# Optimization experiments

Hardware: AMD Instinct MI355X
Metric: run time of the kernel (lower is better)

## Reference

```python
import jax, jax.numpy as jnp
import numpy as np

B, R, L = 1, 128, 256
IN_DIM, DM, DIM = 128, 32, 128  # in_dim, dim_msa, dim


def setup_inputs() -> dict:
    key = jax.random.key(0)
    k = jax.random.split(key, 6)
    x = jax.random.normal(k[0], (B, L, L, DIM), dtype=jnp.float32)
    m = jax.random.normal(k[1], (B, R, L, IN_DIM), dtype=jnp.float32)
    # proj_down1: Linear(in_dim -> dim_msa)
    W1 = jax.random.normal(k[2], (DM, IN_DIM), dtype=jnp.float32) * (1.0 / np.sqrt(IN_DIM))
    b1 = jax.random.normal(k[3], (DM,), dtype=jnp.float32) * 0.02
    # proj_down2: Linear(dim_msa**2 -> dim)
    W2 = jax.random.normal(k[4], (DIM, DM * DM), dtype=jnp.float32) * (1.0 / DM)
    b2 = jax.random.normal(k[5], (DIM,), dtype=jnp.float32) * 0.02
    return {"x": x, "m": m, "W1": W1, "b1": b1, "W2": W2, "b2": b2}


def reference(x, m, W1, b1, W2, b2):
    # proj_down1: [b, r, i, in_dim] -> [b, r, i, dim_msa]
    mp = jnp.einsum('brie,de->brid', m, W1) + b1
    nrows = mp.shape[1]
    # Original math: outer = einsum('brid,brjc->bijcd', mp, mp)/nrows,
    # then rearrange 'b i j c d -> b i j (c d)' and Linear(dm^2 -> dim).
    # Flattened index (c d) => W2[k, c*DM + d]; fuse projection into the
    # contraction so the huge [b,i,j,c,d] tensor is never materialized.
    W2r = W2.reshape(DIM, DM, DM)  # (k, c, d)
    outer = jnp.einsum('brid,brjc,kcd->bijk', mp, mp, W2r) / nrows + b2
    return x + outer
```

## Files before the change

kernel.cpp:

```cpp
#include <hip/hip_runtime.h>
#include <stdint.h>


typedef __attribute__((ext_vector_type(8))) short bf16x8;
typedef __attribute__((ext_vector_type(4))) float f32x4;

#define MFMA16 __builtin_amdgcn_mfma_f32_16x16x32_bf16

__device__ __forceinline__ unsigned short f2bf(float f) {
    union { float f; unsigned int u; } x; x.f = f;
    unsigned int r = (x.u + 0x7fffu + ((x.u >> 16) & 1u)) >> 16;
    return (unsigned short)r;
}

__device__ __forceinline__ bf16x8 load8f_bf(const float* p) {
    float4 v0 = *(const float4*)p;
    float4 v1 = *(const float4*)(p + 4);
    union { bf16x8 v; unsigned short u[8]; } r;
    r.u[0] = f2bf(v0.x); r.u[1] = f2bf(v0.y); r.u[2] = f2bf(v0.z); r.u[3] = f2bf(v0.w);
    r.u[4] = f2bf(v1.x); r.u[5] = f2bf(v1.y); r.u[6] = f2bf(v1.z); r.u[7] = f2bf(v1.w);
    return r.v;
}

__global__ __launch_bounds__(256) void prep_kernel(
    const float* __restrict__ m, const float* __restrict__ W1,
    const float* __restrict__ pb1, const float* __restrict__ W2,
    unsigned short* __restrict__ mpF, unsigned short* __restrict__ W2f)
{
    const int bx = blockIdx.x;
    if (bx >= 512) {
        const int t    = (bx - 512) * 256 + threadIdx.x;
        const int nt   = t >> 11;
        const int kc   = (t >> 6) & 31;
        const int lane = t & 63;
        const int ln   = lane & 15, q = lane >> 4;
        const float* src = W2 + (size_t)(nt * 16 + ln) * 1024 + kc;
        union { bf16x8 v; unsigned short u[8]; } r;
        #pragma unroll
        for (int j = 0; j < 8; ++j)
            r.u[j] = f2bf(src[(q * 8 + j) * 32]);
        *(bf16x8*)(W2f + (size_t)t * 8) = r.v;
        return;
    }
    const int lane = threadIdx.x & 63;
    const int w    = threadIdx.x >> 6;
    const int ln   = lane & 15, q = lane >> 4;
    const int tile = bx * 4 + w;
    const int i    = tile >> 3;
    const int r0   = (tile & 7) * 16;

    const float* Ap  = m  + ((size_t)(r0 + ln) * 256 + i) * 128 + q * 8;
    const float* Bp0 = W1 + (size_t)ln * 128 + q * 8;
    const float* Bp1 = W1 + (size_t)(16 + ln) * 128 + q * 8;

    f32x4 acc0 = {0.f, 0.f, 0.f, 0.f};
    f32x4 acc1 = {0.f, 0.f, 0.f, 0.f};
    #pragma unroll
    for (int ke = 0; ke < 4; ++ke) {
        bf16x8 a  = load8f_bf(Ap  + ke * 32);
        bf16x8 b0 = load8f_bf(Bp0 + ke * 32);
        bf16x8 b1 = load8f_bf(Bp1 + ke * 32);
        acc0 = MFMA16(a, b0, acc0, 0, 0, 0);
        acc1 = MFMA16(a, b1, acc1, 0, 0, 0);
    }
    const float bb0 = pb1[ln];
    const float bb1 = pb1[16 + ln];
    const int kr = r0 >> 5;
    const int qr = ((r0 >> 4) & 1) * 2 + (q >> 1);
    const int j0 = (q & 1) * 4;
    const size_t off0 = (size_t)(i * 2 + 0) * 2048 + kr * 512 + (qr * 16 + ln) * 8 + j0;
    const size_t off1 = (size_t)(i * 2 + 1) * 2048 + kr * 512 + (qr * 16 + ln) * 8 + j0;
    ushort4 o0, o1;
    o0.x = f2bf(acc0[0] + bb0); o0.y = f2bf(acc0[1] + bb0);
    o0.z = f2bf(acc0[2] + bb0); o0.w = f2bf(acc0[3] + bb0);
    o1.x = f2bf(acc1[0] + bb1); o1.y = f2bf(acc1[1] + bb1);
    o1.z = f2bf(acc1[2] + bb1); o1.w = f2bf(acc1[3] + bb1);
    *(ushort4*)(mpF + off0) = o0;
    *(ushort4*)(mpF + off1) = o1;
}

__device__ __forceinline__ void stepB(const unsigned short* __restrict__ Ab,
                                      const unsigned short* __restrict__ Bb,
                                      f32x4 (&acc)[2][4])
{
    #pragma unroll
    for (int a = 0; a < 2; ++a)
        #pragma unroll
        for (int b = 0; b < 4; ++b)
            acc[a][b] = (f32x4){0.f, 0.f, 0.f, 0.f};
    #pragma unroll
    for (int ks = 0; ks < 4; ++ks) {
        bf16x8 av[2], bv[4];
        av[0] = *(const bf16x8*)(Ab + ks * 512);
        av[1] = *(const bf16x8*)(Ab + 2048 + ks * 512);
        #pragma unroll
        for (int bn = 0; bn < 4; ++bn)
            bv[bn] = *(const bf16x8*)(Bb + bn * 4096 + ks * 512);
        #pragma unroll
        for (int am = 0; am < 2; ++am)
            #pragma unroll
            for (int bn = 0; bn < 4; ++bn)
                acc[am][bn] = MFMA16(av[am], bv[bn], acc[am][bn], 0, 0, 0);
    }
}

__device__ __forceinline__ void gwriteC(unsigned short* __restrict__ Gl,
                                        const f32x4 (&acc)[2][4],
                                        int ln, int q, int wm, int wn, int cbase)
{
    #pragma unroll
    for (int am = 0; am < 2; ++am) {
        const int chunk = cbase + ln * 4 + am * 2 + (q >> 1);
        const int sig   = chunk >> 3;
        const int hbase = chunk * 256 + (q & 1) * 4;
        #pragma unroll
        for (int bn = 0; bn < 4; ++bn) {
            const int p  = (wn * 4 + bn) * 4 + wm;
            const int pp = p ^ sig;
            ushort4 g;
            g.x = f2bf(acc[am][bn][0]); g.y = f2bf(acc[am][bn][1]);
            g.z = f2bf(acc[am][bn][2]); g.w = f2bf(acc[am][bn][3]);
            *(ushort4*)(Gl + hbase + pp * 8) = g;
        }
    }
}

__device__ __forceinline__ void wpre(const unsigned short* __restrict__ wp, bf16x8 (&wv)[8])
{
    #pragma unroll
    for (int k8 = 0; k8 < 8; ++k8)
        wv[k8] = *(const bf16x8*)(wp + k8 * 512);
}

__device__ __forceinline__ void stepC32(const unsigned short* __restrict__ Gl,
                                        const unsigned short* __restrict__ wp,
                                        bf16x8 (&wv)[8], int ln, int q,
                                        f32x4& c0, f32x4& c1)
{
    #pragma unroll
    for (int ks = 0; ks < 32; ++ks) {
        bf16x8 cur = wv[ks & 7];
        if (ks < 24) wv[ks & 7] = *(const bf16x8*)(wp + (ks + 8) * 512);
        const int chunk = ks * 4 + q;
        const int sig   = chunk >> 3;
        const unsigned short* gp = Gl + chunk * 256 + ((ln ^ sig) << 3);
        bf16x8 ag0 = *(const bf16x8*)gp;
        bf16x8 ag1 = *(const bf16x8*)(gp + 128);
        c0 = MFMA16(ag0, cur, c0, 0, 0, 0);
        c1 = MFMA16(ag1, cur, c1, 0, 0, 0);
    }
}

__global__ __launch_bounds__(512, 4) void fused_kernel(
    const float* __restrict__ x, const float* __restrict__ b2,
    const unsigned short* __restrict__ mpF, const unsigned short* __restrict__ W2f,
    float* __restrict__ out)
{
    __shared__ __align__(16) unsigned char smem[65536];
    unsigned short* Gl = (unsigned short*)smem;

    const int tid  = threadIdx.x;
    const int lane = tid & 63, w = tid >> 6;
    const int ln   = lane & 15, q = lane >> 4;
    const int wm   = w & 3, wn = w >> 2;

    const int i0 = blockIdx.x * 8;
    const int j0 = blockIdx.y * 8;

    const unsigned short* Ab0 = mpF + (size_t)((j0 + wm) * 2) * 2048 + lane * 8;
    const unsigned short* Ab1 = Ab0 + 16384;
    const unsigned short* Bb  = mpF + (size_t)((i0 + wn * 4) * 2) * 2048 + lane * 8;
    const unsigned short* wp0 = W2f + (size_t)(w * 32) * 512 + lane * 8;

    f32x4 cacc[4];
    #pragma unroll
    for (int t = 0; t < 4; ++t) cacc[t] = (f32x4){0.f, 0.f, 0.f, 0.f};
    f32x4 acc[2][4];
    bf16x8 wv[8];

    stepB(Ab0, Bb, acc);
    gwriteC(Gl, acc, ln, q, wm, wn, 0);
    stepB(Ab0, Bb + 2048, acc);
    gwriteC(Gl, acc, ln, q, wm, wn, 64);
    wpre(wp0, wv);
    __syncthreads();
    stepC32(Gl, wp0, wv, ln, q, cacc[0], cacc[1]);
    __syncthreads();

    stepB(Ab1, Bb, acc);
    gwriteC(Gl, acc, ln, q, wm, wn, 0);
    stepB(Ab1, Bb + 2048, acc);
    gwriteC(Gl, acc, ln, q, wm, wn, 64);
    wpre(wp0, wv);
    __syncthreads();

    float4 xv[4];
    size_t gb[4];
    #pragma unroll
    for (int e = 0; e < 4; ++e) {
        const int fid = e * 512 + tid;
        const int po  = fid >> 5, kq = fid & 31;
        gb[e] = ((size_t)(i0 + (po >> 3)) * 256 + (j0 + (po & 7))) * 128 + kq * 4;
        xv[e] = *(const float4*)(x + gb[e]);
    }

    stepC32(Gl, wp0, wv, ln, q, cacc[2], cacc[3]);
    __syncthreads();

    float* Ep = (float*)smem;
    const float invR = 1.0f / 128.0f;
    const int kk = w * 16 + ln;
    const int u  = kk >> 2, kl = kk & 3;
    #pragma unroll
    for (int jh = 0; jh < 2; ++jh)
        #pragma unroll
        for (int pt = 0; pt < 2; ++pt)
            #pragma unroll
            for (int rg = 0; rg < 4; ++rg) {
                const int po = (pt * 4 + q) * 8 + jh * 4 + rg;
                Ep[po * 128 + ((u ^ (po & 7)) << 2) + kl] = cacc[jh * 2 + pt][rg] * invR;
            }
    __syncthreads();

    #pragma unroll
    for (int e = 0; e < 4; ++e) {
        const int fid = e * 512 + tid;
        const int po  = fid >> 5, kq = fid & 31;
        const float4 v  = *(const float4*)(Ep + po * 128 + ((kq ^ (po & 7)) << 2));
        const float4 bv = *(const float4*)(b2 + kq * 4);
        float4 o;
        o.x = xv[e].x + v.x + bv.x; o.y = xv[e].y + v.y + bv.y;
        o.z = xv[e].z + v.z + bv.z; o.w = xv[e].w + v.w + bv.w;
        *(float4*)(out + gb[e]) = o;
    }
}

extern "C" void kernel_launch(void* const* d_in, const int* in_sizes, int n_in,
                              void* d_out, int out_size, void* d_ws, size_t ws_size,
                              hipStream_t stream) {
    const float* x  = (const float*)d_in[0];
    const float* m  = (const float*)d_in[1];
    const float* W1 = (const float*)d_in[2];
    const float* b1 = (const float*)d_in[3];
    const float* W2 = (const float*)d_in[4];
    const float* b2 = (const float*)d_in[5];
    float* out = (float*)d_out;

    unsigned short* mpF = (unsigned short*)d_ws;
    unsigned short* W2f = mpF + (size_t)512 * 2048;

    prep_kernel<<<dim3(576), dim3(256), 0, stream>>>(m, W1, b1, W2, mpF, W2f);
    fused_kernel<<<dim3(32, 32), dim3(512), 0, stream>>>(x, b2, mpF, W2f, out);
}
```

Baseline: 158.4 us.

## Repartition stage-C work so each warp reuses G fragments across two W2 tiles

Reassigns the second-stage GEMM so each warp owns two 16-wide output column tiles and half of the j range, instead of one column tile across both halves. Each loaded G fragment from LDS now feeds four MFMAs instead of two, which halves LDS reads per MFMA. The phase order changes so both i-halves for a given j-half are produced before consumption. The register-ring W2 prefetch is replaced by direct per-step loads, which risks exposing global/L2 latency on the weight fetches.

New measurement: 162.3 us. 2.4% more time.

```diff
diff --git a/kernel.cpp b/kernel.cpp
--- a/kernel.cpp
+++ b/kernel.cpp
@@ -125,29 +125,25 @@
     }
 }
 
-__device__ __forceinline__ void wpre(const unsigned short* __restrict__ wp, bf16x8 (&wv)[8])
-{
-    #pragma unroll
-    for (int k8 = 0; k8 < 8; ++k8)
-        wv[k8] = *(const bf16x8*)(wp + k8 * 512);
-}
-
-__device__ __forceinline__ void stepC32(const unsigned short* __restrict__ Gl,
-                                        const unsigned short* __restrict__ wp,
-                                        bf16x8 (&wv)[8], int ln, int q,
-                                        f32x4& c0, f32x4& c1)
-{
-    #pragma unroll
-    for (int ks = 0; ks < 32; ++ks) {
-        bf16x8 cur = wv[ks & 7];
-        if (ks < 24) wv[ks & 7] = *(const bf16x8*)(wp + (ks + 8) * 512);
-        const int chunk = ks * 4 + q;
+__device__ __forceinline__ void stepC2(const unsigned short* __restrict__ Gl,
+                                       const unsigned short* __restrict__ wpA,
+                                       const unsigned short* __restrict__ wpB,
+                                       int cb, int ln, int q,
+                                       f32x4& c0, f32x4& c1, f32x4& c2, f32x4& c3)
+{
+    #pragma unroll
+    for (int ks = 0; ks < 16; ++ks) {
+        bf16x8 wa = *(const bf16x8*)(wpA + ks * 512);
+        bf16x8 wb = *(const bf16x8*)(wpB + ks * 512);
+        const int chunk = cb + ks * 4 + q;
         const int sig   = chunk >> 3;
         const unsigned short* gp = Gl + chunk * 256 + ((ln ^ sig) << 3);
         bf16x8 ag0 = *(const bf16x8*)gp;
         bf16x8 ag1 = *(const bf16x8*)(gp + 128);
-        c0 = MFMA16(ag0, cur, c0, 0, 0, 0);
-        c1 = MFMA16(ag1, cur, c1, 0, 0, 0);
+        c0 = MFMA16(ag0, wa, c0, 0, 0, 0);
+        c1 = MFMA16(ag1, wa, c1, 0, 0, 0);
+        c2 = MFMA16(ag0, wb, c2, 0, 0, 0);
+        c3 = MFMA16(ag1, wb, c3, 0, 0, 0);
     }
 }
 
@@ -170,28 +166,29 @@
     const unsigned short* Ab0 = mpF + (size_t)((j0 + wm) * 2) * 2048 + lane * 8;
     const unsigned short* Ab1 = Ab0 + 16384;
     const unsigned short* Bb  = mpF + (size_t)((i0 + wn * 4) * 2) * 2048 + lane * 8;
-    const unsigned short* wp0 = W2f + (size_t)(w * 32) * 512 + lane * 8;
+
+    const int jh = w >> 2;
+    const int cb = jh * 64;
+    const unsigned short* wpA = W2f + (size_t)((w & 3) * 2) * 16384 + lane * 8;
+    const unsigned short* wpB = wpA + 16384;
 
     f32x4 cacc[4];
     #pragma unroll
     for (int t = 0; t < 4; ++t) cacc[t] = (f32x4){0.f, 0.f, 0.f, 0.f};
     f32x4 acc[2][4];
-    bf16x8 wv[8];
 
     stepB(Ab0, Bb, acc);
     gwriteC(Gl, acc, ln, q, wm, wn, 0);
+    stepB(Ab1, Bb, acc);
+    gwriteC(Gl, acc, ln, q, wm, wn, 64);
+    __syncthreads();
+    stepC2(Gl, wpA, wpB, cb, ln, q, cacc[0], cacc[1], cacc[2], cacc[3]);
+    __syncthreads();
+
     stepB(Ab0, Bb + 2048, acc);
-    gwriteC(Gl, acc, ln, q, wm, wn, 64);
-    wpre(wp0, wv);
-    __syncthreads();
-    stepC32(Gl, wp0, wv, ln, q, cacc[0], cacc[1]);
-    __syncthreads();
-
-    stepB(Ab1, Bb, acc);
     gwriteC(Gl, acc, ln, q, wm, wn, 0);
     stepB(Ab1, Bb + 2048, acc);
     gwriteC(Gl, acc, ln, q, wm, wn, 64);
-    wpre(wp0, wv);
     __syncthreads();
 
     float4 xv[4];
@@ -204,22 +201,23 @@
         xv[e] = *(const float4*)(x + gb[e]);
     }
 
-    stepC32(Gl, wp0, wv, ln, q, cacc[2], cacc[3]);
+    stepC2(Gl, wpA + 8192, wpB + 8192, cb, ln, q, cacc[0], cacc[1], cacc[2], cacc[3]);
     __syncthreads();
 
     float* Ep = (float*)smem;
     const float invR = 1.0f / 128.0f;
-    const int kk = w * 16 + ln;
-    const int u  = kk >> 2, kl = kk & 3;
-    #pragma unroll
-    for (int jh = 0; jh < 2; ++jh)
+    #pragma unroll
+    for (int s = 0; s < 2; ++s) {
+        const int kk = ((w & 3) * 2 + s) * 16 + ln;
+        const int u  = kk >> 2, kl = kk & 3;
         #pragma unroll
         for (int pt = 0; pt < 2; ++pt)
             #pragma unroll
             for (int rg = 0; rg < 4; ++rg) {
                 const int po = (pt * 4 + q) * 8 + jh * 4 + rg;
-                Ep[po * 128 + ((u ^ (po & 7)) << 2) + kl] = cacc[jh * 2 + pt][rg] * invR;
+                Ep[po * 128 + ((u ^ (po & 7)) << 2) + kl] = cacc[s * 2 + pt][rg] * invR;
             }
+    }
     __syncthreads();
 
     #pragma unroll
```

## Switch second contraction to 32x32 MFMA with split-K accumulation and direct epilogue

Applied to the files above, without the earlier changes.

Reorganizes the second GEMM stage so each wave uses 32x32x16 bf16 MFMA over a c-split of the reduction, accumulating into a single 16-float fragment across two halves. The W2 pre-packing and the shared-memory layout of the intermediate G are reordered to match, and the LDS transpose epilogue is replaced by direct scalar global stores of x+result+bias. It also adds s_setprio around the MFMA blocks. This cuts LDS traffic and a barrier, but the output stores become strided 4-byte accesses rather than coalesced float4 writes.

New measurement: 333.7 us. 111% more time.

```diff
diff --git a/kernel.cpp b/kernel.cpp
--- a/kernel.cpp
+++ b/kernel.cpp
@@ -4,8 +4,10 @@
 
 typedef __attribute__((ext_vector_type(8))) short bf16x8;
 typedef __attribute__((ext_vector_type(4))) float f32x4;
+typedef __attribute__((ext_vector_type(16))) float f32x16;
 
 #define MFMA16 __builtin_amdgcn_mfma_f32_16x16x32_bf16
+#define MFMA32 __builtin_amdgcn_mfma_f32_32x32x16_bf16
 
 __device__ __forceinline__ unsigned short f2bf(float f) {
     union { float f; unsigned int u; } x; x.f = f;
@@ -30,15 +32,18 @@
     const int bx = blockIdx.x;
     if (bx >= 512) {
         const int t    = (bx - 512) * 256 + threadIdx.x;
-        const int nt   = t >> 11;
-        const int kc   = (t >> 6) & 31;
+        const int kt2  = t >> 12;
+        const int g16  = (t >> 6) & 63;
         const int lane = t & 63;
-        const int ln   = lane & 15, q = lane >> 4;
-        const float* src = W2 + (size_t)(nt * 16 + ln) * 1024 + kc;
+        const int l31  = lane & 31, h = lane >> 5;
+        const int kout = kt2 * 32 + l31;
         union { bf16x8 v; unsigned short u[8]; } r;
         #pragma unroll
-        for (int j = 0; j < 8; ++j)
-            r.u[j] = f2bf(src[(q * 8 + j) * 32]);
+        for (int j = 0; j < 8; ++j) {
+            const int cd = g16 * 16 + h * 8 + j;
+            const int c  = cd & 31, d = cd >> 5;
+            r.u[j] = f2bf(W2[(size_t)kout * 1024 + c * 32 + d]);
+        }
         *(bf16x8*)(W2f + (size_t)t * 8) = r.v;
         return;
     }
@@ -96,23 +101,25 @@
         #pragma unroll
         for (int bn = 0; bn < 4; ++bn)
             bv[bn] = *(const bf16x8*)(Bb + bn * 4096 + ks * 512);
+        __builtin_amdgcn_s_setprio(1);
         #pragma unroll
         for (int am = 0; am < 2; ++am)
             #pragma unroll
             for (int bn = 0; bn < 4; ++bn)
                 acc[am][bn] = MFMA16(av[am], bv[bn], acc[am][bn], 0, 0, 0);
-    }
-}
-
-__device__ __forceinline__ void gwriteC(unsigned short* __restrict__ Gl,
+        __builtin_amdgcn_s_setprio(0);
+    }
+}
+
+__device__ __forceinline__ void gwriteJ(unsigned short* __restrict__ Gl,
                                         const f32x4 (&acc)[2][4],
-                                        int ln, int q, int wm, int wn, int cbase)
+                                        int ln, int q, int wm, int wn, int sbase)
 {
     #pragma unroll
     for (int am = 0; am < 2; ++am) {
-        const int chunk = cbase + ln * 4 + am * 2 + (q >> 1);
+        const int chunk = ln * 4 + am * 2 + (q >> 1);
         const int sig   = chunk >> 3;
-        const int hbase = chunk * 256 + (q & 1) * 4;
+        const int hbase = chunk * 512 + sbase * 8 + (q & 1) * 4;
         #pragma unroll
         for (int bn = 0; bn < 4; ++bn) {
             const int p  = (wn * 4 + bn) * 4 + wm;
@@ -134,20 +141,20 @@
 
 __device__ __forceinline__ void stepC32(const unsigned short* __restrict__ Gl,
                                         const unsigned short* __restrict__ wp,
-                                        bf16x8 (&wv)[8], int ln, int q,
-                                        f32x4& c0, f32x4& c1)
-{
-    #pragma unroll
-    for (int ks = 0; ks < 32; ++ks) {
-        bf16x8 cur = wv[ks & 7];
-        if (ks < 24) wv[ks & 7] = *(const bf16x8*)(wp + (ks + 8) * 512);
-        const int chunk = ks * 4 + q;
-        const int sig   = chunk >> 3;
-        const unsigned short* gp = Gl + chunk * 256 + ((ln ^ sig) << 3);
-        bf16x8 ag0 = *(const bf16x8*)gp;
-        bf16x8 ag1 = *(const bf16x8*)(gp + 128);
-        c0 = MFMA16(ag0, cur, c0, 0, 0, 0);
-        c1 = MFMA16(ag1, cur, c1, 0, 0, 0);
+                                        bf16x8 (&wv)[8], int l31, int h, int jh,
+                                        f32x16& c)
+{
+    #pragma unroll
+    for (int t = 0; t < 32; ++t) {
+        bf16x8 cur = wv[t & 7];
+        if (t < 24) wv[t & 7] = *(const bf16x8*)(wp + (t + 8) * 512);
+        const int g   = t * 2 + h;
+        const int sig = g >> 3;
+        const unsigned short* gp = Gl + g * 512 + ((jh * 32 + (l31 ^ sig)) << 3);
+        bf16x8 ag = *(const bf16x8*)gp;
+        __builtin_amdgcn_s_setprio(1);
+        c = MFMA32(ag, cur, c, 0, 0, 0);
+        __builtin_amdgcn_s_setprio(0);
     }
 }
 
@@ -163,6 +170,8 @@
     const int lane = tid & 63, w = tid >> 6;
     const int ln   = lane & 15, q = lane >> 4;
     const int wm   = w & 3, wn = w >> 2;
+    const int l31  = lane & 31, h = lane >> 5;
+    const int kt2  = w & 3, jh = w >> 2;
 
     const int i0 = blockIdx.x * 8;
     const int j0 = blockIdx.y * 8;
@@ -170,68 +179,51 @@
     const unsigned short* Ab0 = mpF + (size_t)((j0 + wm) * 2) * 2048 + lane * 8;
     const unsigned short* Ab1 = Ab0 + 16384;
     const unsigned short* Bb  = mpF + (size_t)((i0 + wn * 4) * 2) * 2048 + lane * 8;
-    const unsigned short* wp0 = W2f + (size_t)(w * 32) * 512 + lane * 8;
-
-    f32x4 cacc[4];
-    #pragma unroll
-    for (int t = 0; t < 4; ++t) cacc[t] = (f32x4){0.f, 0.f, 0.f, 0.f};
+    const unsigned short* wp0 = W2f + (size_t)(kt2 * 64) * 512 + lane * 8;
+
+    f32x16 cacc;
+    #pragma unroll
+    for (int t = 0; t < 16; ++t) cacc[t] = 0.f;
     f32x4 acc[2][4];
     bf16x8 wv[8];
 
     stepB(Ab0, Bb, acc);
-    gwriteC(Gl, acc, ln, q, wm, wn, 0);
-    stepB(Ab0, Bb + 2048, acc);
-    gwriteC(Gl, acc, ln, q, wm, wn, 64);
+    gwriteJ(Gl, acc, ln, q, wm, wn, 0);
+    stepB(Ab1, Bb, acc);
+    gwriteJ(Gl, acc, ln, q, wm, wn, 32);
     wpre(wp0, wv);
     __syncthreads();
-    stepC32(Gl, wp0, wv, ln, q, cacc[0], cacc[1]);
+    stepC32(Gl, wp0, wv, l31, h, jh, cacc);
+    __builtin_amdgcn_sched_barrier(0);
     __syncthreads();
 
-    stepB(Ab1, Bb, acc);
-    gwriteC(Gl, acc, ln, q, wm, wn, 0);
+    stepB(Ab0, Bb + 2048, acc);
+    gwriteJ(Gl, acc, ln, q, wm, wn, 0);
     stepB(Ab1, Bb + 2048, acc);
-    gwriteC(Gl, acc, ln, q, wm, wn, 64);
-    wpre(wp0, wv);
+    gwriteJ(Gl, acc, ln, q, wm, wn, 32);
+    wpre(wp0 + 16384, wv);
     __syncthreads();
 
-    float4 xv[4];
-    size_t gb[4];
-    #pragma unroll
-    for (int e = 0; e < 4; ++e) {
-        const int fid = e * 512 + tid;
-        const int po  = fid >> 5, kq = fid & 31;
-        gb[e] = ((size_t)(i0 + (po >> 3)) * 256 + (j0 + (po & 7))) * 128 + kq * 4;
-        xv[e] = *(const float4*)(x + gb[e]);
-    }
-
-    stepC32(Gl, wp0, wv, ln, q, cacc[2], cacc[3]);
-    __syncthreads();
-
-    float* Ep = (float*)smem;
+    const int kout = kt2 * 32 + l31;
+    const float bb = b2[kout];
+    float xv16[16];
+    #pragma unroll
+    for (int r = 0; r < 16; ++r) {
+        const int pair = (r & 3) + 8 * (r >> 2) + 4 * h;
+        const size_t addr =
+            ((size_t)(i0 + (pair >> 2)) * 256 + (j0 + jh * 4 + (pair & 3))) * 128 + kout;
+        xv16[r] = x[addr];
+    }
+
+    stepC32(Gl, wp0 + 16384, wv, l31, h, jh, cacc);
+
     const float invR = 1.0f / 128.0f;
-    const int kk = w * 16 + ln;
-    const int u  = kk >> 2, kl = kk & 3;
-    #pragma unroll
-    for (int jh = 0; jh < 2; ++jh)
-        #pragma unroll
-        for (int pt = 0; pt < 2; ++pt)
-            #pragma unroll
-            for (int rg = 0; rg < 4; ++rg) {
-                const int po = (pt * 4 + q) * 8 + jh * 4 + rg;
-                Ep[po * 128 + ((u ^ (po & 7)) << 2) + kl] = cacc[jh * 2 + pt][rg] * invR;
-            }
-    __syncthreads();
-
-    #pragma unroll
-    for (int e = 0; e < 4; ++e) {
-        const int fid = e * 512 + tid;
-        const int po  = fid >> 5, kq = fid & 31;
-        const float4 v  = *(const float4*)(Ep + po * 128 + ((kq ^ (po & 7)) << 2));
-        const float4 bv = *(const float4*)(b2 + kq * 4);
-        float4 o;
-        o.x = xv[e].x + v.x + bv.x; o.y = xv[e].y + v.y + bv.y;
-        o.z = xv[e].z + v.z + bv.z; o.w = xv[e].w + v.w + bv.w;
-        *(float4*)(out + gb[e]) = o;
+    #pragma unroll
+    for (int r = 0; r < 16; ++r) {
+        const int pair = (r & 3) + 8 * (r >> 2) + 4 * h;
+        const size_t addr =
+            ((size_t)(i0 + (pair >> 2)) * 256 + (j0 + jh * 4 + (pair & 3))) * 128 + kout;
+        out[addr] = xv16[r] + cacc[r] * invR + bb;
     }
 }
 
```
